# Kernel tuning notes

Hardware: AMD Instinct MI355X
Metric: run time of the kernel (lower is better)

## Reference

```python
import jax, jax.numpy as jnp
import numpy as np

N = 50000      # nodes
E = 400000     # edges (before self-loops)
IN = 128       # in_channels
OUT = 64       # out_channels (per-head; concat=False averages heads)
HEADS = 8      # heads of first GAT layer; second layer has 1 head
NEG_SLOPE = 0.2


def _glorot(key, shape, fan_in, fan_out):
    s = jnp.sqrt(2.0 / (fan_in + fan_out)).astype(jnp.float32)
    return jax.random.normal(key, shape, jnp.float32) * s


def setup_inputs() -> dict:
    key = jax.random.key(0)
    ks = jax.random.split(key, 10)
    x = jax.random.normal(ks[0], (N, IN), jnp.float32)
    edge_index = jax.random.randint(ks[1], (2, E), 0, N)
    # layer 1: heads=HEADS, per-head dim OUT
    W1 = _glorot(ks[2], (IN, HEADS * OUT), IN, HEADS * OUT)
    att_src1 = _glorot(ks[3], (HEADS, OUT), OUT, 1)
    att_dst1 = _glorot(ks[4], (HEADS, OUT), OUT, 1)
    b1 = jnp.zeros((OUT,), jnp.float32)
    # layer 2: heads=1
    W2 = _glorot(ks[5], (OUT, 1 * OUT), OUT, OUT)
    att_src2 = _glorot(ks[6], (1, OUT), OUT, 1)
    att_dst2 = _glorot(ks[7], (1, OUT), OUT, 1)
    b2 = jnp.zeros((OUT,), jnp.float32)
    return dict(x=x, edge_index=edge_index, W1=W1, att_src1=att_src1,
                att_dst1=att_dst1, b1=b1, W2=W2, att_src2=att_src2,
                att_dst2=att_dst2, b2=b2)


def gat_conv(x, edge_index, W, att_src, att_dst, bias, heads, ch):
    """PyG GATConv with concat=False (mean over heads), add_self_loops=True."""
    n = x.shape[0]
    loop = jnp.arange(n, dtype=edge_index.dtype)
    src = jnp.concatenate([edge_index[0], loop])  # [E+N]
    dst = jnp.concatenate([edge_index[1], loop])
    h = (x @ W).reshape(n, heads, ch)                     # [N, H, C]
    a_s = jnp.sum(h * att_src, axis=-1)                   # [N, H]
    a_d = jnp.sum(h * att_dst, axis=-1)                   # [N, H]
    e = jax.nn.leaky_relu(a_s[src] + a_d[dst], NEG_SLOPE)  # [E+N, H]
    # numerically stable segment softmax over incoming edges of each dst node
    emax = jax.lax.stop_gradient(
        jax.ops.segment_max(e, dst, num_segments=n))       # [N, H]
    ee = jnp.exp(e - emax[dst])
    denom = jax.ops.segment_sum(ee, dst, num_segments=n)  # [N, H]
    alpha = ee / denom[dst]                                # [E+N, H]
    out = jax.ops.segment_sum(alpha[:, :, None] * h[src], dst,
                              num_segments=n)              # [N, H, C]
    return out.mean(axis=1) + bias                         # [N, C]


def reference(x, edge_index, W1, att_src1, att_dst1, b1,
              W2, att_src2, att_dst2, b2):
    h = gat_conv(x, edge_index, W1, att_src1, att_dst1, b1, HEADS, OUT)
    h = jax.nn.elu(h)
    return gat_conv(h, edge_index, W2, att_src2, att_dst2, b2, 1, OUT)
```

## Files before the change

kernel.cpp:

```cpp
#include <hip/hip_runtime.h>
#include <cstdint>
#include <cstddef>

#define NEG_SLOPE 0.2f

typedef short bf16x8 __attribute__((ext_vector_type(8)));
typedef float f32x4 __attribute__((ext_vector_type(4)));
typedef float f32x2 __attribute__((ext_vector_type(2)));

__device__ __forceinline__ unsigned short f2bf(float f) {
  unsigned u = __float_as_uint(f);
  u = u + 0x7FFFu + ((u >> 16) & 1u);
  return (unsigned short)(u >> 16);
}
__device__ __forceinline__ float bf2f(unsigned short b) {
  return __uint_as_float((unsigned)b << 16);
}
__device__ __forceinline__ f32x2 unpk(unsigned xv) {
  f32x2 r;
  r.x = __uint_as_float(xv << 16);
  r.y = __uint_as_float(xv & 0xFFFF0000u);
  return r;
}

__global__ __launch_bounds__(256) void prep_all(
    const int* __restrict__ ei, int* __restrict__ counts,
    const float* __restrict__ x, unsigned short* __restrict__ xb,
    const float* __restrict__ W1, const float* __restrict__ att_s1,
    const float* __restrict__ att_d1, unsigned short* __restrict__ AsAdT,
    unsigned short* __restrict__ WbT,
    const float* __restrict__ W2, unsigned short* __restrict__ W2t,
    const float* __restrict__ att_s2, const float* __restrict__ att_d2,
    float* __restrict__ AsAd2,
    int E, int ET, int N, int B0, int B1) {
  int b = blockIdx.x, tid = threadIdx.x;
  if (b < B0) {
    int i = b * 256 + tid;
    if (i < ET) {
      int dst = (i < E) ? ei[E + i] : (i - E);
      atomicAdd(&counts[dst], 1);
    }
    return;
  }
  b -= B0;
  if (b < B1) {
    int i = b * 256 + tid;
    if (i < N * 32) {
      float4 v = ((const float4*)x)[i];
      ushort4 o;
      o.x = f2bf(v.x); o.y = f2bf(v.y); o.z = f2bf(v.z); o.w = f2bf(v.w);
      ((ushort4*)xb)[i] = o;
    }
    return;
  }
  b -= B1;
  if (b < 8) {
    int i = b * 256 + tid;
    int o = i >> 7, k = i & 127, h = o & 7;
    const float* att = (o < 8) ? att_s1 : att_d1;
    float s = 0.f;
    for (int c = 0; c < 64; c++) s += W1[(size_t)k * 512 + h * 64 + c] * att[h * 64 + c];
    AsAdT[i] = f2bf(s);
    return;
  }
  b -= 8;
  if (b < 256) {
    int i = b * 256 + tid;
    int o = i >> 10, k = i & 1023, h = k >> 7, c = k & 127;
    WbT[i] = f2bf(W1[(size_t)c * 512 + h * 64 + o]);
    return;
  }
  b -= 256;
  if (b < 16) {
    int i = b * 256 + tid;
    if (i < 64 * 64) {
      int k = i >> 6, nn = i & 63;
      W2t[(size_t)nn * 64 + k] = f2bf(W2[i]);
    }
    return;
  }
  {
    int i = tid;
    if (i < 128) {
      int o = i >> 6, k = i & 63;
      const float* att = (o == 0) ? att_s2 : att_d2;
      float s = 0.f;
      for (int c = 0; c < 64; c++) s += W2[(size_t)k * 64 + c] * att[c];
      AsAd2[i] = s;
    }
  }
}

__global__ __launch_bounds__(1024) void scan_dots(
    const int* __restrict__ counts, int* __restrict__ offsets,
    const unsigned short* __restrict__ xb, const unsigned short* __restrict__ AsAdT,
    float* __restrict__ asd, int n) {
  if (blockIdx.x == 0) {
    __shared__ int sums[1024];
    int t = threadIdx.x;
    int chunk = (n + 1023) >> 10;
    int start = t * chunk;
    int end = min(start + chunk, n);
    int s = 0;
    for (int i = start; i < end; i++) s += counts[i];
    sums[t] = s;
    __syncthreads();
    for (int off = 1; off < 1024; off <<= 1) {
      int v = (t >= off) ? sums[t - off] : 0;
      __syncthreads();
      sums[t] += v;
      __syncthreads();
    }
    int run = sums[t] - s;
    for (int i = start; i < end; i++) { offsets[i] = run; run += counts[i]; }
    if (t == 1023) offsets[n] = sums[1023];
    return;
  }
  int tid = threadIdx.x;
  int wave = tid >> 6, lane = tid & 63;
  int q = lane >> 4, t = lane & 15;
  int row0 = (blockIdx.x - 1) * 256 + wave * 16;
  int arow = row0 + t; if (arow > n - 1) arow = n - 1;
  const bf16x8* aptr = (const bf16x8*)(xb + (size_t)arow * 128);
  const bf16x8* bptr = (const bf16x8*)(AsAdT + t * 128);
  f32x4 acc = (f32x4){0.f, 0.f, 0.f, 0.f};
  #pragma unroll
  for (int s = 0; s < 4; s++)
    acc = __builtin_amdgcn_mfma_f32_16x16x32_bf16(aptr[s * 4 + q], bptr[s * 4 + q],
                                                  acc, 0, 0, 0);
  #pragma unroll
  for (int r = 0; r < 4; r++) {
    int row = row0 + q * 4 + r;
    if (row < n) asd[row * 16 + t] = acc[r];
  }
}

__global__ __launch_bounds__(256) void fill_weights(
    const int* __restrict__ ei, const int* __restrict__ offsets,
    int* __restrict__ cursor, int* __restrict__ srcs,
    const float* __restrict__ asd, float* __restrict__ wbuf,
    int E, int ET) {
  int i = blockIdx.x * 256 + threadIdx.x;
  if (i >= ET) return;
  int src, dst;
  if (i < E) { src = ei[i]; dst = ei[E + i]; } else { src = dst = i - E; }
  int pos = atomicAdd(&cursor[dst], 1);
  int slot = offsets[dst] + pos;
  srcs[slot] = src;
  float4 s0 = *(const float4*)&asd[src * 16];
  float4 s1 = *(const float4*)&asd[src * 16 + 4];
  float4 d0 = *(const float4*)&asd[dst * 16 + 8];
  float4 d1 = *(const float4*)&asd[dst * 16 + 12];
  float w[8];
  w[0] = s0.x + d0.x; w[1] = s0.y + d0.y; w[2] = s0.z + d0.z; w[3] = s0.w + d0.w;
  w[4] = s1.x + d1.x; w[5] = s1.y + d1.y; w[6] = s1.z + d1.z; w[7] = s1.w + d1.w;
  #pragma unroll
  for (int h = 0; h < 8; h++) {
    float v = w[h];
    v = (v > 0.f) ? v : NEG_SLOPE * v;
    w[h] = __expf(v);
  }
  float4* wp = (float4*)&wbuf[(size_t)slot * 8];
  wp[0] = make_float4(w[0], w[1], w[2], w[3]);
  wp[1] = make_float4(w[4], w[5], w[6], w[7]);
}

__global__ __launch_bounds__(1024, 8) void agg1_gemm(
    const int* __restrict__ offsets, const int* __restrict__ srcs,
    const float* __restrict__ wbuf, const unsigned short* __restrict__ xb,
    const unsigned short* __restrict__ WbT, const float* __restrict__ b1,
    const float* __restrict__ AsAd2, unsigned short* __restrict__ zb,
    float* __restrict__ as2, float* __restrict__ ad2, int N) {
  __shared__ unsigned short sh[16 * 1032];
  __shared__ float sas[16], sad[16];
  int tid = threadIdx.x;
  int wv = tid >> 6, lane = tid & 63;
  int nb = blockIdx.x;
  {
    int row = wv;
    int node = nb * 16 + row;
    float2 acc[8];
    float ws[8];
    #pragma unroll
    for (int h = 0; h < 8; h++) { acc[h].x = 0.f; acc[h].y = 0.f; ws[h] = 0.f; }
    int beg = offsets[node], end = offsets[node + 1];
    int jl = end - 1;
    int s_cur = srcs[beg];
    int jn1 = (beg + 1 <= jl) ? beg + 1 : jl;
    int s_nxt = srcs[jn1];
    float4 wa_p = *(const float4*)&wbuf[(size_t)beg * 8];
    float4 wb_p = *(const float4*)&wbuf[(size_t)beg * 8 + 4];
    unsigned xv_p = *(const unsigned*)&xb[(size_t)s_cur * 128 + 2 * lane];
    for (int j = beg; j < end; j++) {
      float4 wa = wa_p, wb = wb_p;
      unsigned xv = xv_p;
      xv_p = *(const unsigned*)&xb[(size_t)s_nxt * 128 + 2 * lane];
      int jn = (j + 1 <= jl) ? j + 1 : jl;
      wa_p = *(const float4*)&wbuf[(size_t)jn * 8];
      wb_p = *(const float4*)&wbuf[(size_t)jn * 8 + 4];
      int jn2 = (j + 2 <= jl) ? j + 2 : jl;
      s_nxt = srcs[jn2];
      float x0 = __uint_as_float(xv << 16);
      float x1 = __uint_as_float(xv & 0xFFFF0000u);
      acc[0].x += wa.x * x0; acc[0].y += wa.x * x1; ws[0] += wa.x;
      acc[1].x += wa.y * x0; acc[1].y += wa.y * x1; ws[1] += wa.y;
      acc[2].x += wa.z * x0; acc[2].y += wa.z * x1; ws[2] += wa.z;
      acc[3].x += wa.w * x0; acc[3].y += wa.w * x1; ws[3] += wa.w;
      acc[4].x += wb.x * x0; acc[4].y += wb.x * x1; ws[4] += wb.x;
      acc[5].x += wb.y * x0; acc[5].y += wb.y * x1; ws[5] += wb.y;
      acc[6].x += wb.z * x0; acc[6].y += wb.z * x1; ws[6] += wb.z;
      acc[7].x += wb.w * x0; acc[7].y += wb.w * x1; ws[7] += wb.w;
    }
    #pragma unroll
    for (int h = 0; h < 8; h++) {
      float iv = 0.125f / ws[h];
      unsigned o = (unsigned)f2bf(acc[h].x * iv) | ((unsigned)f2bf(acc[h].y * iv) << 16);
      *(unsigned*)&sh[row * 1032 + h * 128 + 2 * lane] = o;
    }
  }
  if (tid < 16) sas[tid] = 0.f;
  else if (tid < 32) sad[tid - 16] = 0.f;
  __syncthreads();
  if (wv < 4) {
    int q = lane >> 4, t = lane & 15;
    f32x4 acc4 = (f32x4){0.f, 0.f, 0.f, 0.f};
    const unsigned short* bbase = WbT + (size_t)(wv * 16 + t) * 1024;
    #pragma unroll 8
    for (int s = 0; s < 32; s++) {
      bf16x8 af = *(const bf16x8*)&sh[t * 1032 + s * 32 + q * 8];
      bf16x8 bf = *(const bf16x8*)&bbase[s * 32 + q * 8];
      acc4 = __builtin_amdgcn_mfma_f32_16x16x32_bf16(af, bf, acc4, 0, 0, 0);
    }
    int col = wv * 16 + t;
    float bias = b1[col];
    float vs = AsAd2[col], vd = AsAd2[64 + col];
    float zr[4];
    #pragma unroll
    for (int r = 0; r < 4; r++) {
      int row = q * 4 + r;
      int node = nb * 16 + row;
      float v = acc4[r] + bias;
      v = (v > 0.f) ? v : (__expf(v) - 1.f);
      zr[r] = v;
      zb[(size_t)node * 64 + col] = f2bf(v);
    }
    #pragma unroll
    for (int r = 0; r < 4; r++) {
      float s = zr[r] * vs, d = zr[r] * vd;
      #pragma unroll
      for (int off = 1; off < 16; off <<= 1) {
        s += __shfl_xor(s, off, 64);
        d += __shfl_xor(d, off, 64);
      }
      if (t == 0) {
        atomicAdd(&sas[q * 4 + r], s);
        atomicAdd(&sad[q * 4 + r], d);
      }
    }
  }
  __syncthreads();
  if (tid < 16) as2[nb * 16 + tid] = sas[tid];
  else if (tid < 32) ad2[nb * 16 + (tid - 16)] = sad[tid - 16];
}

__global__ __launch_bounds__(1024, 8) void agg2_gemm(
    const int* __restrict__ offsets, const int* __restrict__ srcs,
    const float* __restrict__ as2, const float* __restrict__ ad2,
    const unsigned short* __restrict__ zb, const unsigned short* __restrict__ W2t,
    const float* __restrict__ b2, float* __restrict__ out, int N) {
  __shared__ unsigned short sh[16 * 72];
  __shared__ int ssrc[16][64];
  int tid = threadIdx.x;
  int wv = tid >> 6, lane = tid & 63;
  int nb = blockIdx.x;
  {
    int row = wv;
    int node = nb * 16 + row;
    int half = lane >> 5;
    int l2 = lane & 31;
    float adv = ad2[node];
    int beg = offsets[node], end = offsets[node + 1];
    f32x2 acc = (f32x2){0.f, 0.f};
    float ws = 0.f;
    for (int cb = beg; cb < end; cb += 64) {
      int cnt = min(64, end - cb);
      if (lane < cnt) ssrc[row][lane] = srcs[cb + lane];
      #pragma unroll 2
      for (int k = half; k < cnt; k += 2) {
        int s = ssrc[row][k];
        float asv = as2[s];
        unsigned zv = *(const unsigned*)&zb[(size_t)s * 64 + 2 * l2];
        float v = asv + adv;
        v = (v > 0.f) ? v : NEG_SLOPE * v;
        float w = __expf(v);
        ws += w;
        acc += unpk(zv) * w;
      }
    }
    acc.x += __shfl_xor(acc.x, 32, 64);
    acc.y += __shfl_xor(acc.y, 32, 64);
    ws += __shfl_xor(ws, 32, 64);
    if (half == 0) {
      float inv = 1.f / ws;
      unsigned o = (unsigned)f2bf(acc.x * inv) | ((unsigned)f2bf(acc.y * inv) << 16);
      *(unsigned*)&sh[row * 72 + 2 * l2] = o;
    }
  }
  __syncthreads();
  if (wv < 4) {
    int q = lane >> 4, t = lane & 15;
    f32x4 acc4 = (f32x4){0.f, 0.f, 0.f, 0.f};
    const unsigned short* bbase = W2t + (size_t)(wv * 16 + t) * 64;
    #pragma unroll
    for (int s = 0; s < 2; s++) {
      bf16x8 af = *(const bf16x8*)&sh[t * 72 + s * 32 + q * 8];
      bf16x8 bf = *(const bf16x8*)&bbase[s * 32 + q * 8];
      acc4 = __builtin_amdgcn_mfma_f32_16x16x32_bf16(af, bf, acc4, 0, 0, 0);
    }
    int col = wv * 16 + t;
    float bias = b2[col];
    #pragma unroll
    for (int r = 0; r < 4; r++) {
      int node = nb * 16 + q * 4 + r;
      if (node < N) out[(size_t)node * 64 + col] = acc4[r] + bias;
    }
  }
}

extern "C" void kernel_launch(void* const* d_in, const int* in_sizes, int n_in,
                              void* d_out, int out_size, void* d_ws, size_t ws_size,
                              hipStream_t stream) {
  const int IN = 128;
  const int N = in_sizes[0] / IN;
  const int E = in_sizes[1] / 2;
  const int ET = E + N;

  const float* x        = (const float*)d_in[0];
  const int*   ei       = (const int*)d_in[1];
  const float* W1       = (const float*)d_in[2];
  const float* att_src1 = (const float*)d_in[3];
  const float* att_dst1 = (const float*)d_in[4];
  const float* b1       = (const float*)d_in[5];
  const float* W2       = (const float*)d_in[6];
  const float* att_src2 = (const float*)d_in[7];
  const float* att_dst2 = (const float*)d_in[8];
  const float* b2       = (const float*)d_in[9];
  float* out = (float*)d_out;

  char* base = (char*)d_ws;
  size_t off = 0;
  auto alloc = [&](size_t bytes) -> char* {
    char* p = base + off;
    off = (off + bytes + 255) & ~(size_t)255;
    return p;
  };
  unsigned short* xb    = (unsigned short*)alloc((size_t)N * 128 * 2);
  unsigned short* AsAdT = (unsigned short*)alloc((size_t)16 * 128 * 2);
  unsigned short* WbT   = (unsigned short*)alloc((size_t)64 * 1024 * 2);
  unsigned short* W2t   = (unsigned short*)alloc((size_t)64 * 64 * 2);
  unsigned short* zb    = (unsigned short*)alloc((size_t)N * 64 * 2);
  float* AsAd2 = (float*)alloc((size_t)128 * 4);
  float* asd1  = (float*)alloc((size_t)N * 16 * 4);
  float* a_s2  = (float*)alloc((size_t)N * 4);
  float* a_d2  = (float*)alloc((size_t)N * 4);
  float* wbuf  = (float*)alloc((size_t)ET * 8 * 4);
  int* offsets = (int*)alloc((size_t)(N + 1) * 4);
  int* srcs    = (int*)alloc((size_t)ET * 4);
  char* zero_begin = base + off;
  int* counts  = (int*)alloc((size_t)N * 4);
  int* cursor  = (int*)alloc((size_t)N * 4);
  char* zero_end = base + off;

  hipMemsetAsync(zero_begin, 0, (size_t)(zero_end - zero_begin), stream);

  const int TB = 256;
  auto cdiv = [](int a, int b) { return (a + b - 1) / b; };

  int B0 = cdiv(ET, TB);
  int B1 = cdiv(N * 32, TB);
  prep_all<<<B0 + B1 + 8 + 256 + 16 + 1, TB, 0, stream>>>(
      ei, counts, x, xb, W1, att_src1, att_dst1, AsAdT, WbT, W2, W2t,
      att_src2, att_dst2, AsAd2, E, ET, N, B0, B1);

  scan_dots<<<1 + cdiv(N, 256), 1024, 0, stream>>>(counts, offsets, xb, AsAdT,
                                                   asd1, N);

  fill_weights<<<cdiv(ET, TB), TB, 0, stream>>>(ei, offsets, cursor, srcs,
                                                asd1, wbuf, E, ET);

  agg1_gemm<<<cdiv(N, 16), 1024, 0, stream>>>(offsets, srcs, wbuf, xb, WbT, b1,
                                              AsAd2, zb, a_s2, a_d2, N);

  agg2_gemm<<<cdiv(N, 16), 1024, 0, stream>>>(offsets, srcs, a_s2, a_d2, zb,
                                              W2t, b2, out, N);
}
```

Measured before the change: 345.0 us.

## Compute edge attention weights inside aggregation instead of materializing per-edge buffer

Removes the per-edge weight buffer (ET×8 floats) that fill_weights wrote, so the CSR fill kernel only scatters source indices. agg1_gemm now loads the per-node source attention logits for each neighbor and the destination logits once, then computes leaky-relu and exp inline. This drops a large write-then-read of edge weights. In exchange every lane of the 64-wide wave recomputes the 8 exps per edge, adding transcendental work to the aggregation loop.

```diff
diff --git a/kernel.cpp b/kernel.cpp
--- a/kernel.cpp
+++ b/kernel.cpp
@@ -21,6 +21,9 @@
   r.x = __uint_as_float(xv << 16);
   r.y = __uint_as_float(xv & 0xFFFF0000u);
   return r;
+}
+__device__ __forceinline__ float wexp(float v) {
+  return __expf(fmaxf(v, NEG_SLOPE * v));
 }
 
 __global__ __launch_bounds__(256) void prep_all(
@@ -135,39 +138,20 @@
   }
 }
 
-__global__ __launch_bounds__(256) void fill_weights(
+__global__ __launch_bounds__(256) void fill_srcs(
     const int* __restrict__ ei, const int* __restrict__ offsets,
-    int* __restrict__ cursor, int* __restrict__ srcs,
-    const float* __restrict__ asd, float* __restrict__ wbuf,
-    int E, int ET) {
+    int* __restrict__ cursor, int* __restrict__ srcs, int E, int ET) {
   int i = blockIdx.x * 256 + threadIdx.x;
   if (i >= ET) return;
   int src, dst;
   if (i < E) { src = ei[i]; dst = ei[E + i]; } else { src = dst = i - E; }
   int pos = atomicAdd(&cursor[dst], 1);
-  int slot = offsets[dst] + pos;
-  srcs[slot] = src;
-  float4 s0 = *(const float4*)&asd[src * 16];
-  float4 s1 = *(const float4*)&asd[src * 16 + 4];
-  float4 d0 = *(const float4*)&asd[dst * 16 + 8];
-  float4 d1 = *(const float4*)&asd[dst * 16 + 12];
-  float w[8];
-  w[0] = s0.x + d0.x; w[1] = s0.y + d0.y; w[2] = s0.z + d0.z; w[3] = s0.w + d0.w;
-  w[4] = s1.x + d1.x; w[5] = s1.y + d1.y; w[6] = s1.z + d1.z; w[7] = s1.w + d1.w;
-  #pragma unroll
-  for (int h = 0; h < 8; h++) {
-    float v = w[h];
-    v = (v > 0.f) ? v : NEG_SLOPE * v;
-    w[h] = __expf(v);
-  }
-  float4* wp = (float4*)&wbuf[(size_t)slot * 8];
-  wp[0] = make_float4(w[0], w[1], w[2], w[3]);
-  wp[1] = make_float4(w[4], w[5], w[6], w[7]);
+  srcs[offsets[dst] + pos] = src;
 }
 
 __global__ __launch_bounds__(1024, 8) void agg1_gemm(
     const int* __restrict__ offsets, const int* __restrict__ srcs,
-    const float* __restrict__ wbuf, const unsigned short* __restrict__ xb,
+    const float* __restrict__ asd, const unsigned short* __restrict__ xb,
     const unsigned short* __restrict__ WbT, const float* __restrict__ b1,
     const float* __restrict__ AsAd2, unsigned short* __restrict__ zb,
     float* __restrict__ as2, float* __restrict__ ad2, int N) {
@@ -183,33 +167,38 @@
     float ws[8];
     #pragma unroll
     for (int h = 0; h < 8; h++) { acc[h].x = 0.f; acc[h].y = 0.f; ws[h] = 0.f; }
+    float4 d0 = *(const float4*)&asd[(size_t)node * 16 + 8];
+    float4 d1 = *(const float4*)&asd[(size_t)node * 16 + 12];
     int beg = offsets[node], end = offsets[node + 1];
     int jl = end - 1;
     int s_cur = srcs[beg];
     int jn1 = (beg + 1 <= jl) ? beg + 1 : jl;
     int s_nxt = srcs[jn1];
-    float4 wa_p = *(const float4*)&wbuf[(size_t)beg * 8];
-    float4 wb_p = *(const float4*)&wbuf[(size_t)beg * 8 + 4];
+    float4 a0_p = *(const float4*)&asd[(size_t)s_cur * 16];
+    float4 a1_p = *(const float4*)&asd[(size_t)s_cur * 16 + 4];
     unsigned xv_p = *(const unsigned*)&xb[(size_t)s_cur * 128 + 2 * lane];
     for (int j = beg; j < end; j++) {
-      float4 wa = wa_p, wb = wb_p;
+      float4 a0 = a0_p, a1 = a1_p;
       unsigned xv = xv_p;
       xv_p = *(const unsigned*)&xb[(size_t)s_nxt * 128 + 2 * lane];
-      int jn = (j + 1 <= jl) ? j + 1 : jl;
-      wa_p = *(const float4*)&wbuf[(size_t)jn * 8];
-      wb_p = *(const float4*)&wbuf[(size_t)jn * 8 + 4];
+      a0_p = *(const float4*)&asd[(size_t)s_nxt * 16];
+      a1_p = *(const float4*)&asd[(size_t)s_nxt * 16 + 4];
       int jn2 = (j + 2 <= jl) ? j + 2 : jl;
       s_nxt = srcs[jn2];
+      float w0 = wexp(a0.x + d0.x), w1 = wexp(a0.y + d0.y);
+      float w2 = wexp(a0.z + d0.z), w3 = wexp(a0.w + d0.w);
+      float w4 = wexp(a1.x + d1.x), w5 = wexp(a1.y + d1.y);
+      float w6 = wexp(a1.z + d1.z), w7 = wexp(a1.w + d1.w);
       float x0 = __uint_as_float(xv << 16);
       float x1 = __uint_as_float(xv & 0xFFFF0000u);
-      acc[0].x += wa.x * x0; acc[0].y += wa.x * x1; ws[0] += wa.x;
-      acc[1].x += wa.y * x0; acc[1].y += wa.y * x1; ws[1] += wa.y;
-      acc[2].x += wa.z * x0; acc[2].y += wa.z * x1; ws[2] += wa.z;
-      acc[3].x += wa.w * x0; acc[3].y += wa.w * x1; ws[3] += wa.w;
-      acc[4].x += wb.x * x0; acc[4].y += wb.x * x1; ws[4] += wb.x;
-      acc[5].x += wb.y * x0; acc[5].y += wb.y * x1; ws[5] += wb.y;
-      acc[6].x += wb.z * x0; acc[6].y += wb.z * x1; ws[6] += wb.z;
-      acc[7].x += wb.w * x0; acc[7].y += wb.w * x1; ws[7] += wb.w;
+      acc[0].x += w0 * x0; acc[0].y += w0 * x1; ws[0] += w0;
+      acc[1].x += w1 * x0; acc[1].y += w1 * x1; ws[1] += w1;
+      acc[2].x += w2 * x0; acc[2].y += w2 * x1; ws[2] += w2;
+      acc[3].x += w3 * x0; acc[3].y += w3 * x1; ws[3] += w3;
+      acc[4].x += w4 * x0; acc[4].y += w4 * x1; ws[4] += w4;
+      acc[5].x += w5 * x0; acc[5].y += w5 * x1; ws[5] += w5;
+      acc[6].x += w6 * x0; acc[6].y += w6 * x1; ws[6] += w6;
+      acc[7].x += w7 * x0; acc[7].y += w7 * x1; ws[7] += w7;
     }
     #pragma unroll
     for (int h = 0; h < 8; h++) {
@@ -363,7 +352,6 @@
   float* asd1  = (float*)alloc((size_t)N * 16 * 4);
   float* a_s2  = (float*)alloc((size_t)N * 4);
   float* a_d2  = (float*)alloc((size_t)N * 4);
-  float* wbuf  = (float*)alloc((size_t)ET * 8 * 4);
   int* offsets = (int*)alloc((size_t)(N + 1) * 4);
   int* srcs    = (int*)alloc((size_t)ET * 4);
   char* zero_begin = base + off;
@@ -385,10 +373,9 @@
   scan_dots<<<1 + cdiv(N, 256), 1024, 0, stream>>>(counts, offsets, xb, AsAdT,
                                                    asd1, N);
 
-  fill_weights<<<cdiv(ET, TB), TB, 0, stream>>>(ei, offsets, cursor, srcs,
-                                                asd1, wbuf, E, ET);
-
-  agg1_gemm<<<cdiv(N, 16), 1024, 0, stream>>>(offsets, srcs, wbuf, xb, WbT, b1,
+  fill_srcs<<<cdiv(ET, TB), TB, 0, stream>>>(ei, offsets, cursor, srcs, E, ET);
+
+  agg1_gemm<<<cdiv(N, 16), 1024, 0, stream>>>(offsets, srcs, asd1, xb, WbT, b1,
                                               AsAd2, zb, a_s2, a_d2, N);
 
   agg2_gemm<<<cdiv(N, 16), 1024, 0, stream>>>(offsets, srcs, a_s2, a_d2, zb,
```

Measured after the change: 360.6 us. +4.5%, slower.
